# Kernel optimization log

Hardware: AMD Instinct MI355X
Metric: run time of the kernel (lower is better)

Reference implementation:

```python
import jax, jax.numpy as jnp
import numpy as np

N, K, D = 65536, 8192, 256

def setup_inputs() -> dict:
    key = jax.random.key(0)
    k1, k2 = jax.random.split(key)
    z = jax.random.normal(k1, (N, D), dtype=jnp.float32)
    # torch init: uniform(-1/K, 1/K)
    emb_w = jax.random.uniform(k2, (K, D), dtype=jnp.float32, minval=-1.0 / K, maxval=1.0 / K)
    return {"z": z, "emb_w": emb_w}

def reference(z, emb_w):
    # distance[n,k] = ||z_n||^2 + ||e_k||^2 - 2 z_n . e_k  (argmin is gradient-free)
    z2 = jnp.sum(z * z, axis=1, keepdims=True)            # [N,1]
    e2 = jnp.sum(emb_w * emb_w, axis=1)                    # [K]
    distance = z2 + e2 - 2.0 * (z @ emb_w.T)               # [N,K]
    indices = jnp.argmin(distance, axis=-1)                # [N]
    quantized = emb_w[indices]                             # [N,D]
    straight_through = jax.lax.stop_gradient(quantized - z) + z
    return quantized, straight_through, indices
```

## Files before the change

### kernel.cpp

```cpp
#include <hip/hip_runtime.h>
#include <hip/hip_fp16.h>

#define N_TOK 65536
#define K_EMB 8192
#define D_DIM 256
#define LIST_CAP 12288
#define CAND_CAP 16384

typedef unsigned short u16;
typedef unsigned int u32;
typedef unsigned long long u64;
typedef _Float16 f16x8 __attribute__((ext_vector_type(8)));
typedef float f32x16 __attribute__((ext_vector_type(16)));

__device__ __forceinline__ u16 f2h(float f) {
  union { _Float16 h; u16 u; } c; c.h = (_Float16)f; return c.u;
}
__device__ __forceinline__ f16x8 as_f16x8(uint4 v) {
  union { uint4 u; f16x8 h; } c; c.u = v; return c.h;
}
__device__ __forceinline__ void gld_lds16(const u16* g, u16* l) {
  __builtin_amdgcn_global_load_lds((const __attribute__((address_space(1))) void*)g,
                                   (__attribute__((address_space(3))) void*)l,
                                   16, 0, 0);
}

__global__ void vq_prep(const float* __restrict__ emb, u16* __restrict__ ehh,
                        float* __restrict__ e2f, u16* __restrict__ e2h,
                        int* __restrict__ count, int* __restrict__ candcount) {
  if (blockIdx.x == 0 && threadIdx.x == 0) { *count = 0; *candcount = 0; }
  const int w = threadIdx.x >> 6, lane = threadIdx.x & 63;
  const int k = blockIdx.x * 4 + w;
  const float4 v = ((const float4*)(emb + (size_t)k * D_DIM))[lane];
  uint2 p;
  p.x = (u32)f2h(v.x * 524288.0f) | ((u32)f2h(v.y * 524288.0f) << 16);
  p.y = (u32)f2h(v.z * 524288.0f) | ((u32)f2h(v.w * 524288.0f) << 16);
  ((uint2*)(ehh + (size_t)k * D_DIM))[lane] = p;
  double s = (double)v.x * v.x + (double)v.y * v.y +
             (double)v.z * v.z + (double)v.w * v.w;
  #pragma unroll
  for (int off = 32; off > 0; off >>= 1) s += __shfl_down(s, off);
  if (lane == 0) { e2f[k] = (float)s; e2h[k] = f2h(-(float)s * 16777216.0f); }
}

__global__ void vq_z2(const float* __restrict__ zg, float* __restrict__ z2f) {
  const int w = threadIdx.x >> 6, lane = threadIdx.x & 63;
  const int n = blockIdx.x * 4 + w;
  const float4 v = ((const float4*)(zg + (size_t)n * D_DIM))[lane];
  double s = (double)v.x * v.x + (double)v.y * v.y +
             (double)v.z * v.z + (double)v.w * v.w;
  #pragma unroll
  for (int off = 32; off > 0; off >>= 1) s += __shfl_down(s, off);
  if (lane == 0) z2f[n] = (float)s;
}

__launch_bounds__(512, 2)
__global__ void vq_phase1(const float* __restrict__ zg, const u16* __restrict__ ehh,
                          const u16* __restrict__ e2h, const float* __restrict__ z2f,
                          int* __restrict__ idx1_ws, int* __restrict__ thrbuf,
                          u64* __restrict__ refbuf, int* __restrict__ list,
                          int* __restrict__ count) {
  __shared__ u16 lds[2][16384];

  const int tid  = threadIdx.x;
  const int w    = tid >> 6;
  const int lane = tid & 63;
  const int q    = w & 1;
  const int g    = w >> 1;
  const int col  = lane & 31;
  const int h    = lane >> 5;
  const int n0   = blockIdx.x * 256 + g * 64;

  uint4 zres[2][16];
  #pragma unroll
  for (int s = 0; s < 2; ++s) {
    const float4* zp = (const float4*)(zg + (size_t)(n0 + s * 32 + col) * D_DIM);
    #pragma unroll
    for (int c = 0; c < 16; ++c) {
      float4 a = zp[c * 4 + h * 2];
      float4 b = zp[c * 4 + h * 2 + 1];
      uint4 u;
      u.x = (u32)f2h(a.x * 64.0f) | ((u32)f2h(a.y * 64.0f) << 16);
      u.y = (u32)f2h(a.z * 64.0f) | ((u32)f2h(a.w * 64.0f) << 16);
      u.z = (u32)f2h(b.x * 64.0f) | ((u32)f2h(b.y * 64.0f) << 16);
      u.w = (u32)f2h(b.z * 64.0f) | ((u32)f2h(b.w * 64.0f) << 16);
      zres[s][c] = u;
    }
  }
  uint4 bone = {0, 0, 0, 0};
  if (h == 0) bone.x = 0x3C00u;

  int m1[2] = {(int)0x80000000, (int)0x80000000};
  int m2[2] = {(int)0x80000000, (int)0x80000000};

  #pragma unroll
  for (int i = 0; i < 4; ++i) {
    int pp = w * 4 + i, qs = pp >> 4, cs = pp & 15;
    gld_lds16(ehh + (size_t)(qs * 32 + col) * D_DIM + cs * 16 + h * 8,
              &lds[0][qs * 8192 + cs * 512]);
  }

  for (int t = 0; t < 128; ++t) {
    const int b = t & 1;
    __syncthreads();
    if (t + 1 < 128) {
      const int nb = b ^ 1, kb2 = (t + 1) * 64;
      #pragma unroll
      for (int i = 0; i < 4; ++i) {
        int pp = w * 4 + i, qs = pp >> 4, cs = pp & 15;
        gld_lds16(ehh + (size_t)(kb2 + qs * 32 + col) * D_DIM + cs * 16 + h * 8,
                  &lds[nb][qs * 8192 + cs * 512]);
      }
    }
    const int kb = t * 64 + q * 32;
    uint4 ea = {0, 0, 0, 0};
    if (h == 0) ea.x = (u32)e2h[kb + col];

    const u16* lb = &lds[b][q * 8192];
    f32x16 acc0 = {}, acc1 = {};
    #pragma unroll
    for (int c = 0; c < 16; ++c) {
      f16x8 a = as_f16x8(*(const uint4*)(lb + c * 512 + lane * 8));
      acc0 = __builtin_amdgcn_mfma_f32_32x32x16_f16(a, as_f16x8(zres[0][c]), acc0, 0, 0, 0);
      acc1 = __builtin_amdgcn_mfma_f32_32x32x16_f16(a, as_f16x8(zres[1][c]), acc1, 0, 0, 0);
    }
    acc0 = __builtin_amdgcn_mfma_f32_32x32x16_f16(as_f16x8(ea), as_f16x8(bone), acc0, 0, 0, 0);
    acc1 = __builtin_amdgcn_mfma_f32_32x32x16_f16(as_f16x8(ea), as_f16x8(bone), acc1, 0, 0, 0);

    const int base_inv = 4095 - t * 32 - q * 16;
    #pragma unroll
    for (int r = 0; r < 16; ++r) {
      {
        int key = ((int)acc0[r] << 12) | (base_inv - r);
        m2[0] = max(m2[0], min(m1[0], key));
        m1[0] = max(m1[0], key);
      }
      {
        int key = ((int)acc1[r] << 12) | (base_inv - r);
        m2[1] = max(m2[1], min(m1[1], key));
        m1[1] = max(m1[1], key);
      }
    }
  }

  int k1[2];
  #pragma unroll
  for (int s = 0; s < 2; ++s) {
    int x = 4095 - (m1[s] & 4095);
    int kt = x >> 5, kq = (x >> 4) & 1, kr = x & 15;
    k1[s] = kt * 64 + kq * 32 + (kr & 3) + 8 * (kr >> 2) + 4 * h;
    int o1 = __shfl_xor(m1[s], 32), o2 = __shfl_xor(m2[s], 32);
    int ok1 = __shfl_xor(k1[s], 32);
    bool take = (o1 > m1[s]) || (o1 == m1[s] && ok1 < k1[s]);
    int loser = take ? m1[s] : o1;
    if (take) { m1[s] = o1; k1[s] = ok1; }
    m2[s] = max(m2[s], max(o2, loser));
  }

  __syncthreads();
  int* rm1 = (int*)&lds[0][0];
  int* rk1 = (int*)&lds[0][1024];
  int* rm2 = (int*)&lds[0][2048];
  if (lane < 32) {
    #pragma unroll
    for (int s = 0; s < 2; ++s) {
      int nl = q * 256 + g * 64 + s * 32 + col;
      rm1[nl] = m1[s]; rk1[nl] = k1[s]; rm2[nl] = m2[s];
    }
  }
  __syncthreads();
  if (tid < 256) {
    int a1 = rm1[tid], a2 = rm2[tid], ak = rk1[tid];
    int c1 = rm1[256 + tid], c2 = rm2[256 + tid], ck = rk1[256 + tid];
    bool take = (c1 > a1) || (c1 == a1 && ck < ak);
    int M1 = take ? c1 : a1;
    int K1 = take ? ck : ak;
    int M2 = max(max(a2, c2), take ? a1 : c1);
    int n = blockIdx.x * 256 + tid;
    int M1a = M1 >> 12, M2a = M2 >> 12;
    int e = (int)((__float_as_uint(z2f[n] + 0.01f) >> 23) & 255);
    e = min(max(e, 127), 140);
    int bin = 1 << (e - 126);
    int p = 0;
    if ((M1a - M2a) < (bin * 2 + 128)) {
      int pos = atomicAdd(count, 1);
      if (pos < LIST_CAP) {
        list[pos] = n;
        thrbuf[pos] = M1a - (bin + 256);
        refbuf[pos] = 0xFFFFFFFFFFFFFFFFULL;
        p = pos + 1;
      }
    }
    idx1_ws[n] = K1 | (p << 13);
  }
}

__launch_bounds__(512, 2)
__global__ void vq_cand(const float* __restrict__ zg, const u16* __restrict__ ehh,
                        const u16* __restrict__ e2h, const int* __restrict__ count,
                        const int* __restrict__ list, const int* __restrict__ thrbuf,
                        u32* __restrict__ candbuf, int* __restrict__ candcount) {
  __shared__ u16 lds[32768];
  int cnt = *count; if (cnt > LIST_CAP) cnt = LIST_CAP;
  const int tile = blockIdx.x;
  if (tile * 64 >= cnt) return;
  const int tid = threadIdx.x, w = tid >> 6, lane = tid & 63;
  const int q = w & 3, g = w >> 2;
  const int col = lane & 31, h = lane >> 5;
  const int ct = tile * 64 + g * 32 + col;
  const bool valid = ct < cnt;
  const int n_tok = valid ? (list[ct] & (N_TOK - 1)) : 0;
  const int thr = valid ? thrbuf[ct] : 0x7FFFFFFF;

  uint4 zres[16];
  {
    const float4* zp = (const float4*)(zg + (size_t)n_tok * D_DIM);
    #pragma unroll
    for (int c = 0; c < 16; ++c) {
      float4 a = zp[c * 4 + h * 2];
      float4 b2 = zp[c * 4 + h * 2 + 1];
      uint4 u;
      u.x = (u32)f2h(a.x * 64.0f) | ((u32)f2h(a.y * 64.0f) << 16);
      u.y = (u32)f2h(a.z * 64.0f) | ((u32)f2h(a.w * 64.0f) << 16);
      u.z = (u32)f2h(b2.x * 64.0f) | ((u32)f2h(b2.y * 64.0f) << 16);
      u.w = (u32)f2h(b2.z * 64.0f) | ((u32)f2h(b2.w * 64.0f) << 16);
      zres[c] = u;
    }
  }
  uint4 bone = {0, 0, 0, 0};
  if (h == 0) bone.x = 0x3C00u;

  for (int tK = 0; tK < 64; ++tK) {
    __syncthreads();
    #pragma unroll
    for (int i = 0; i < 8; ++i) {
      int p2 = w * 8 + i, qs = p2 >> 4, cs = p2 & 15;
      gld_lds16(ehh + (size_t)(tK * 128 + qs * 32 + col) * D_DIM + cs * 16 + h * 8,
                &lds[qs * 8192 + cs * 512]);
    }
    __syncthreads();
    const int kb = tK * 128 + q * 32;
    uint4 ea = {0, 0, 0, 0};
    if (h == 0) ea.x = (u32)e2h[kb + col];
    const u16* lb = &lds[q * 8192];
    f32x16 acc = {};
    #pragma unroll
    for (int c = 0; c < 16; ++c) {
      f16x8 a = as_f16x8(*(const uint4*)(lb + c * 512 + lane * 8));
      acc = __builtin_amdgcn_mfma_f32_32x32x16_f16(a, as_f16x8(zres[c]), acc, 0, 0, 0);
    }
    acc = __builtin_amdgcn_mfma_f32_32x32x16_f16(as_f16x8(ea), as_f16x8(bone), acc, 0, 0, 0);
    #pragma unroll
    for (int r = 0; r < 16; ++r) {
      if ((int)acc[r] >= thr) {
        int kg = kb + (r & 3) + 8 * (r >> 2) + 4 * h;
        int pos = atomicAdd(candcount, 1);
        if (pos < CAND_CAP) candbuf[pos] = ((u32)ct << 13) | (u32)kg;
      }
    }
  }
}

__global__ void vq_refine2(const float* __restrict__ zg, const float* __restrict__ emb,
                           const float* __restrict__ z2f, const float* __restrict__ e2f,
                           const int* __restrict__ list, const int* __restrict__ candcount,
                           const u32* __restrict__ candbuf, u64* __restrict__ refbuf) {
  const int w = threadIdx.x >> 6, lane = threadIdx.x & 63;
  int ccnt = *candcount; if (ccnt > CAND_CAP) ccnt = CAND_CAP;
  for (int i = blockIdx.x * 4 + w; i < ccnt; i += gridDim.x * 4) {
    const u32 rec = candbuf[i];
    const int p = (int)(rec >> 13), k = (int)(rec & 8191u);
    const int n = list[p] & (N_TOK - 1);
    float4 zv = ((const float4*)(zg + (size_t)n * D_DIM))[lane];
    float4 ev = ((const float4*)(emb + (size_t)k * D_DIM))[lane];
    double s = (double)zv.x * ev.x + (double)zv.y * ev.y +
               (double)zv.z * ev.z + (double)zv.w * ev.w;
    #pragma unroll
    for (int off = 32; off > 0; off >>= 1) s += __shfl_down(s, off);
    if (lane == 0) {
      float S = z2f[n] + e2f[k];
      float val = S - 2.0f * (float)s;
      u64 key = ((u64)__float_as_uint(val) << 13) | (u64)k;
      atomicMin((unsigned long long*)(refbuf + p), (unsigned long long)key);
    }
  }
}

__global__ void vq_gather(const float* __restrict__ emb, const int* __restrict__ idx1_ws,
                          const u64* __restrict__ refbuf, float* __restrict__ out) {
  const int w = threadIdx.x >> 6, lane = threadIdx.x & 63;
  const int n = blockIdx.x * 4 + w;
  const int enc = idx1_ws[n];
  int idx = enc & 8191;
  const int p = enc >> 13;
  if (p > 0) {
    u64 rb = refbuf[p - 1];
    if (rb != 0xFFFFFFFFFFFFFFFFULL) idx = (int)(rb & 8191ULL);
  }
  float4 v = ((const float4*)(emb + (size_t)idx * D_DIM))[lane];
  float4* o = (float4*)out;
  o[(size_t)n * 64 + lane] = v;
  o[(size_t)4194304 + (size_t)n * 64 + lane] = v;
  if (lane == 0) out[(size_t)33554432 + n] = (float)idx;
}

extern "C" void kernel_launch(void* const* d_in, const int* in_sizes, int n_in,
                              void* d_out, int out_size, void* d_ws, size_t ws_size,
                              hipStream_t stream) {
  const float* z   = (const float*)d_in[0];
  const float* emb = (const float*)d_in[1];
  char* ws = (char*)d_ws;
  u16*   ehh       = (u16*)(ws);
  float* e2f       = (float*)(ws + 4194304);
  u16*   e2h       = (u16*)(ws + 4227072);
  float* z2f       = (float*)(ws + 4243456);
  int*   idx1_ws   = (int*)(ws + 4505600);
  u64*   refbuf    = (u64*)(ws + 4767744);
  int*   list      = (int*)(ws + 4866048);
  int*   thrbuf    = (int*)(ws + 4915200);
  u32*   candbuf   = (u32*)(ws + 4964352);
  int*   count     = (int*)(ws + 5029888);
  int*   candcount = (int*)(ws + 5029892);

  vq_prep   <<<K_EMB / 4, 256, 0, stream>>>(emb, ehh, e2f, e2h, count, candcount);
  vq_z2     <<<N_TOK / 4, 256, 0, stream>>>(z, z2f);
  vq_phase1 <<<N_TOK / 256, 512, 0, stream>>>(z, ehh, e2h, z2f, idx1_ws, thrbuf,
                                              refbuf, list, count);
  vq_cand   <<<256, 512, 0, stream>>>(z, ehh, e2h, count, list, thrbuf,
                                      candbuf, candcount);
  vq_refine2<<<256, 256, 0, stream>>>(z, emb, z2f, e2f, list, candcount,
                                      candbuf, refbuf);
  vq_gather <<<N_TOK / 4, 256, 0, stream>>>(emb, idx1_ws, refbuf, (float*)d_out);
}
```

Baseline: 755.3 us.

## Halve phase1 token tile for higher occupancy and double-buffer vq_cand LDS loads

```diff
diff --git a/kernel.cpp b/kernel.cpp
--- a/kernel.cpp
+++ b/kernel.cpp
@@ -54,7 +54,7 @@
   if (lane == 0) z2f[n] = (float)s;
 }
 
-__launch_bounds__(512, 2)
+__launch_bounds__(512, 4)
 __global__ void vq_phase1(const float* __restrict__ zg, const u16* __restrict__ ehh,
                           const u16* __restrict__ e2h, const float* __restrict__ z2f,
                           int* __restrict__ idx1_ws, int* __restrict__ thrbuf,
@@ -69,12 +69,11 @@
   const int g    = w >> 1;
   const int col  = lane & 31;
   const int h    = lane >> 5;
-  const int n0   = blockIdx.x * 256 + g * 64;
-
-  uint4 zres[2][16];
-  #pragma unroll
-  for (int s = 0; s < 2; ++s) {
-    const float4* zp = (const float4*)(zg + (size_t)(n0 + s * 32 + col) * D_DIM);
+  const int n0   = blockIdx.x * 128 + g * 32;
+
+  uint4 zres[16];
+  {
+    const float4* zp = (const float4*)(zg + (size_t)(n0 + col) * D_DIM);
     #pragma unroll
     for (int c = 0; c < 16; ++c) {
       float4 a = zp[c * 4 + h * 2];
@@ -84,14 +83,13 @@
       u.y = (u32)f2h(a.z * 64.0f) | ((u32)f2h(a.w * 64.0f) << 16);
       u.z = (u32)f2h(b.x * 64.0f) | ((u32)f2h(b.y * 64.0f) << 16);
       u.w = (u32)f2h(b.z * 64.0f) | ((u32)f2h(b.w * 64.0f) << 16);
-      zres[s][c] = u;
+      zres[c] = u;
     }
   }
   uint4 bone = {0, 0, 0, 0};
   if (h == 0) bone.x = 0x3C00u;
 
-  int m1[2] = {(int)0x80000000, (int)0x80000000};
-  int m2[2] = {(int)0x80000000, (int)0x80000000};
+  int m1 = (int)0x80000000, m2 = (int)0x80000000;
 
   #pragma unroll
   for (int i = 0; i < 4; ++i) {
@@ -117,44 +115,34 @@
     if (h == 0) ea.x = (u32)e2h[kb + col];
 
     const u16* lb = &lds[b][q * 8192];
-    f32x16 acc0 = {}, acc1 = {};
+    f32x16 acc = {};
     #pragma unroll
     for (int c = 0; c < 16; ++c) {
       f16x8 a = as_f16x8(*(const uint4*)(lb + c * 512 + lane * 8));
-      acc0 = __builtin_amdgcn_mfma_f32_32x32x16_f16(a, as_f16x8(zres[0][c]), acc0, 0, 0, 0);
-      acc1 = __builtin_amdgcn_mfma_f32_32x32x16_f16(a, as_f16x8(zres[1][c]), acc1, 0, 0, 0);
-    }
-    acc0 = __builtin_amdgcn_mfma_f32_32x32x16_f16(as_f16x8(ea), as_f16x8(bone), acc0, 0, 0, 0);
-    acc1 = __builtin_amdgcn_mfma_f32_32x32x16_f16(as_f16x8(ea), as_f16x8(bone), acc1, 0, 0, 0);
+      acc = __builtin_amdgcn_mfma_f32_32x32x16_f16(a, as_f16x8(zres[c]), acc, 0, 0, 0);
+    }
+    acc = __builtin_amdgcn_mfma_f32_32x32x16_f16(as_f16x8(ea), as_f16x8(bone), acc, 0, 0, 0);
 
     const int base_inv = 4095 - t * 32 - q * 16;
     #pragma unroll
     for (int r = 0; r < 16; ++r) {
-      {
-        int key = ((int)acc0[r] << 12) | (base_inv - r);
-        m2[0] = max(m2[0], min(m1[0], key));
-        m1[0] = max(m1[0], key);
-      }
-      {
-        int key = ((int)acc1[r] << 12) | (base_inv - r);
-        m2[1] = max(m2[1], min(m1[1], key));
-        m1[1] = max(m1[1], key);
-      }
-    }
-  }
-
-  int k1[2];
-  #pragma unroll
-  for (int s = 0; s < 2; ++s) {
-    int x = 4095 - (m1[s] & 4095);
+      int key = ((int)acc[r] << 12) + (base_inv - r);
+      m2 = max(m2, min(m1, key));
+      m1 = max(m1, key);
+    }
+  }
+
+  int k1;
+  {
+    int x = 4095 - (m1 & 4095);
     int kt = x >> 5, kq = (x >> 4) & 1, kr = x & 15;
-    k1[s] = kt * 64 + kq * 32 + (kr & 3) + 8 * (kr >> 2) + 4 * h;
-    int o1 = __shfl_xor(m1[s], 32), o2 = __shfl_xor(m2[s], 32);
-    int ok1 = __shfl_xor(k1[s], 32);
-    bool take = (o1 > m1[s]) || (o1 == m1[s] && ok1 < k1[s]);
-    int loser = take ? m1[s] : o1;
-    if (take) { m1[s] = o1; k1[s] = ok1; }
-    m2[s] = max(m2[s], max(o2, loser));
+    k1 = kt * 64 + kq * 32 + (kr & 3) + 8 * (kr >> 2) + 4 * h;
+    int o1 = __shfl_xor(m1, 32), o2 = __shfl_xor(m2, 32);
+    int ok1 = __shfl_xor(k1, 32);
+    bool take = (o1 > m1) || (o1 == m1 && ok1 < k1);
+    int loser = take ? m1 : o1;
+    if (take) { m1 = o1; k1 = ok1; }
+    m2 = max(m2, max(o2, loser));
   }
 
   __syncthreads();
@@ -162,21 +150,18 @@
   int* rk1 = (int*)&lds[0][1024];
   int* rm2 = (int*)&lds[0][2048];
   if (lane < 32) {
-    #pragma unroll
-    for (int s = 0; s < 2; ++s) {
-      int nl = q * 256 + g * 64 + s * 32 + col;
-      rm1[nl] = m1[s]; rk1[nl] = k1[s]; rm2[nl] = m2[s];
-    }
+    int nl = q * 128 + g * 32 + col;
+    rm1[nl] = m1; rk1[nl] = k1; rm2[nl] = m2;
   }
   __syncthreads();
-  if (tid < 256) {
+  if (tid < 128) {
     int a1 = rm1[tid], a2 = rm2[tid], ak = rk1[tid];
-    int c1 = rm1[256 + tid], c2 = rm2[256 + tid], ck = rk1[256 + tid];
+    int c1 = rm1[128 + tid], c2 = rm2[128 + tid], ck = rk1[128 + tid];
     bool take = (c1 > a1) || (c1 == a1 && ck < ak);
     int M1 = take ? c1 : a1;
     int K1 = take ? ck : ak;
     int M2 = max(max(a2, c2), take ? a1 : c1);
-    int n = blockIdx.x * 256 + tid;
+    int n = blockIdx.x * 128 + tid;
     int M1a = M1 >> 12, M2a = M2 >> 12;
     int e = (int)((__float_as_uint(z2f[n] + 0.01f) >> 23) & 255);
     e = min(max(e, 127), 140);
@@ -200,7 +185,7 @@
                         const u16* __restrict__ e2h, const int* __restrict__ count,
                         const int* __restrict__ list, const int* __restrict__ thrbuf,
                         u32* __restrict__ candbuf, int* __restrict__ candcount) {
-  __shared__ u16 lds[32768];
+  __shared__ u16 lds[2][32768];
   int cnt = *count; if (cnt > LIST_CAP) cnt = LIST_CAP;
   const int tile = blockIdx.x;
   if (tile * 64 >= cnt) return;
@@ -230,19 +215,29 @@
   uint4 bone = {0, 0, 0, 0};
   if (h == 0) bone.x = 0x3C00u;
 
+  #pragma unroll
+  for (int i = 0; i < 8; ++i) {
+    int p2 = w * 8 + i, qs = p2 >> 4, cs = p2 & 15;
+    gld_lds16(ehh + (size_t)(qs * 32 + col) * D_DIM + cs * 16 + h * 8,
+              &lds[0][qs * 8192 + cs * 512]);
+  }
+
   for (int tK = 0; tK < 64; ++tK) {
+    const int b = tK & 1;
     __syncthreads();
-    #pragma unroll
-    for (int i = 0; i < 8; ++i) {
-      int p2 = w * 8 + i, qs = p2 >> 4, cs = p2 & 15;
-      gld_lds16(ehh + (size_t)(tK * 128 + qs * 32 + col) * D_DIM + cs * 16 + h * 8,
-                &lds[qs * 8192 + cs * 512]);
-    }
-    __syncthreads();
+    if (tK + 1 < 64) {
+      const int nb = b ^ 1, kb2 = (tK + 1) * 128;
+      #pragma unroll
+      for (int i = 0; i < 8; ++i) {
+        int p2 = w * 8 + i, qs = p2 >> 4, cs = p2 & 15;
+        gld_lds16(ehh + (size_t)(kb2 + qs * 32 + col) * D_DIM + cs * 16 + h * 8,
+                  &lds[nb][qs * 8192 + cs * 512]);
+      }
+    }
     const int kb = tK * 128 + q * 32;
     uint4 ea = {0, 0, 0, 0};
     if (h == 0) ea.x = (u32)e2h[kb + col];
-    const u16* lb = &lds[q * 8192];
+    const u16* lb = &lds[b][q * 8192];
     f32x16 acc = {};
     #pragma unroll
     for (int c = 0; c < 16; ++c) {
@@ -324,7 +319,7 @@
 
   vq_prep   <<<K_EMB / 4, 256, 0, stream>>>(emb, ehh, e2f, e2h, count, candcount);
   vq_z2     <<<N_TOK / 4, 256, 0, stream>>>(z, z2f);
-  vq_phase1 <<<N_TOK / 256, 512, 0, stream>>>(z, ehh, e2h, z2f, idx1_ws, thrbuf,
+  vq_phase1 <<<N_TOK / 128, 512, 0, stream>>>(z, ehh, e2h, z2f, idx1_ws, thrbuf,
                                               refbuf, list, count);
   vq_cand   <<<256, 512, 0, stream>>>(z, ehh, e2h, count, list, thrbuf,
                                       candbuf, candcount);
```

Measured after the change: 742.4 us. Within noise of the previous version (-1.7%).
